# Performance work log

Hardware: AMD Instinct MI355X
Metric: run time of the kernel (lower is better)

Reference implementation:

```python
import jax, jax.numpy as jnp
import numpy as np

N, E, F, H, ED, C, G = 50000, 800000, 86, 128, 16, 18, 64
NEG_SLOPE = 0.2


def setup_inputs() -> dict:
    key = jax.random.key(0)
    ks = jax.random.split(key, 20)
    s = 0.1
    return {
        "x": jax.random.normal(ks[0], (N, F), jnp.float32),
        "edge_index": jax.random.randint(ks[1], (2, E), 0, N, jnp.int32),
        "edge_attr": jax.random.normal(ks[2], (E, ED), jnp.float32),
        "batch": jnp.sort(jax.random.randint(ks[3], (N,), 0, G, jnp.int32)),
        # conv1 params (GATConv, heads=1): lin, lin_edge (no bias), att vectors, bias
        "W1": jax.random.normal(ks[4], (F, H), jnp.float32) * s,
        "We1": jax.random.normal(ks[5], (ED, H), jnp.float32) * s,
        "as1": jax.random.normal(ks[6], (H,), jnp.float32) * s,
        "ad1": jax.random.normal(ks[7], (H,), jnp.float32) * s,
        "ae1": jax.random.normal(ks[8], (H,), jnp.float32) * s,
        "b1": jnp.zeros((H,), jnp.float32),
        # conv2 params
        "W2": jax.random.normal(ks[9], (H, H), jnp.float32) * s,
        "We2": jax.random.normal(ks[10], (ED, H), jnp.float32) * s,
        "as2": jax.random.normal(ks[11], (H,), jnp.float32) * s,
        "ad2": jax.random.normal(ks[12], (H,), jnp.float32) * s,
        "ae2": jax.random.normal(ks[13], (H,), jnp.float32) * s,
        "b2": jnp.zeros((H,), jnp.float32),
        # final classifier
        "Wl": jax.random.normal(ks[14], (H, C), jnp.float32) * s,
        "bl": jnp.zeros((C,), jnp.float32),
    }


def gat_conv(x, edge_attr, src, dst, W, We, a_src, a_dst, a_edge, bias):
    h = x @ W                                   # [N, H]
    e = edge_attr @ We                          # [E, H]
    # per-edge attention logits: a_src.h_j + a_dst.h_i + a_edge.e
    alpha = (h @ a_src)[src] + (h @ a_dst)[dst] + e @ a_edge   # [E]
    alpha = jax.nn.leaky_relu(alpha, NEG_SLOPE)
    # segment softmax over incoming edges of each destination node
    m = jax.ops.segment_max(alpha, dst, num_segments=N)
    ex = jnp.exp(alpha - m[dst])
    denom = jax.ops.segment_sum(ex, dst, num_segments=N)
    w = ex / jnp.maximum(denom[dst], 1e-16)     # [E]
    out = jax.ops.segment_sum(h[src] * w[:, None], dst, num_segments=N)
    return out + bias


def reference(x, edge_index, edge_attr, batch,
              W1, We1, as1, ad1, ae1, b1,
              W2, We2, as2, ad2, ae2, b2,
              Wl, bl):
    src, dst = edge_index[0], edge_index[1]
    h = jax.nn.relu(gat_conv(x, edge_attr, src, dst, W1, We1, as1, ad1, ae1, b1))
    h = jax.nn.relu(gat_conv(h, edge_attr, src, dst, W2, We2, as2, ad2, ae2, b2))
    pooled = jax.ops.segment_max(h, batch, num_segments=G)      # [G, H] global max pool
    pooled = jnp.where(jnp.isfinite(pooled), pooled, 0.0)       # guard empty graphs
    logits = pooled @ Wl + bl                                   # [G, C]
    return jax.nn.log_softmax(logits, axis=-1)
```

## Files before the change

kernel.cpp:

```cpp
#include <hip/hip_runtime.h>
#include <math.h>

#define N_NODES 50000
#define N_EDGES 800000
#define F_IN    86
#define H_DIM   128
#define ED_DIM  16
#define C_CLS   18
#define G_GRAPHS 64
#define NEG_SLOPE 0.2f
#define SCAN_BLOCKS ((N_NODES + 255) / 256)
#define EB_BLOCKS ((N_EDGES + 255) / 256)
#define GB_BLOCKS ((N_NODES + 63) / 64)

typedef _Float16 h2v   __attribute__((ext_vector_type(2)));
typedef _Float16 half8 __attribute__((ext_vector_type(8)));
typedef float    f4v   __attribute__((ext_vector_type(4)));

__device__ __forceinline__ void atomicMaxFloat(float* addr, float val) {
    if (val >= 0.0f) atomicMax((int*)addr, __float_as_int(val));
    else             atomicMin((unsigned int*)addr, __float_as_uint(val));
}

__global__ void prep(int* __restrict__ cnt, float* __restrict__ pooled,
                     const float* __restrict__ We1, const float* __restrict__ ae1,
                     const float* __restrict__ We2, const float* __restrict__ ae2,
                     float* __restrict__ ve1, float* __restrict__ ve2) {
    int b = blockIdx.x, t = threadIdx.x;
    if (b < SCAN_BLOCKS) {
        int i = b * 256 + t;
        if (i < N_NODES) cnt[i] = 0;
    } else {
        if (t < ED_DIM) {
            float s = 0.f;
            for (int h = 0; h < H_DIM; ++h) s += We1[t * H_DIM + h] * ae1[h];
            ve1[t] = s;
        } else if (t < 2 * ED_DIM) {
            int j = t - ED_DIM;
            float s = 0.f;
            for (int h = 0; h < H_DIM; ++h) s += We2[j * H_DIM + h] * ae2[h];
            ve2[j] = s;
        }
        for (int i = t; i < G_GRAPHS * H_DIM; i += 256) pooled[i] = 0.f;
    }
}

__global__ void hist_rank_dots(const int* __restrict__ dst, int* __restrict__ cnt,
                               unsigned short* __restrict__ rank,
                               const float* __restrict__ ea,
                               const float* __restrict__ ve1, const float* __restrict__ ve2,
                               unsigned int* __restrict__ dotp) {
    int e = blockIdx.x * blockDim.x + threadIdx.x;
    if (e >= N_EDGES) return;
    int r = atomicAdd(&cnt[dst[e]], 1);
    rank[e] = (unsigned short)r;
    const float4* p = (const float4*)(ea + (size_t)e * ED_DIM);
    float4 v0 = p[0], v1 = p[1], v2 = p[2], v3 = p[3];
    float s1 = v0.x*ve1[0] + v0.y*ve1[1] + v0.z*ve1[2] + v0.w*ve1[3]
             + v1.x*ve1[4] + v1.y*ve1[5] + v1.z*ve1[6] + v1.w*ve1[7]
             + v2.x*ve1[8] + v2.y*ve1[9] + v2.z*ve1[10] + v2.w*ve1[11]
             + v3.x*ve1[12] + v3.y*ve1[13] + v3.z*ve1[14] + v3.w*ve1[15];
    float s2 = v0.x*ve2[0] + v0.y*ve2[1] + v0.z*ve2[2] + v0.w*ve2[3]
             + v1.x*ve2[4] + v1.y*ve2[5] + v1.z*ve2[6] + v1.w*ve2[7]
             + v2.x*ve2[8] + v2.y*ve2[9] + v2.z*ve2[10] + v2.w*ve2[11]
             + v3.x*ve2[12] + v3.y*ve2[13] + v3.z*ve2[14] + v3.w*ve2[15];
    h2v dv;
    dv.x = (_Float16)s1;
    dv.y = (_Float16)s2;
    dotp[e] = __builtin_bit_cast(unsigned int, dv);
}

__global__ void scan1(const int* __restrict__ cnt, int* __restrict__ excl,
                      int* __restrict__ bsum) {
    __shared__ int s[256];
    int tid = threadIdx.x;
    int i = blockIdx.x * 256 + tid;
    int v = (i < N_NODES) ? cnt[i] : 0;
    s[tid] = v;
    __syncthreads();
    for (int o = 1; o < 256; o <<= 1) {
        int t = (tid >= o) ? s[tid - o] : 0;
        __syncthreads();
        s[tid] += t;
        __syncthreads();
    }
    if (i < N_NODES) excl[i] = s[tid] - v;
    if (tid == 255) bsum[blockIdx.x] = s[255];
}

__global__ void scan23(const int* __restrict__ excl, const int* __restrict__ bsum,
                       int* __restrict__ row_ptr) {
    __shared__ int s[256];
    int tid = threadIdx.x;
    int v = (tid < SCAN_BLOCKS) ? bsum[tid] : 0;
    s[tid] = v;
    __syncthreads();
    for (int o = 1; o < 256; o <<= 1) {
        int t = (tid >= o) ? s[tid - o] : 0;
        __syncthreads();
        s[tid] += t;
        __syncthreads();
    }
    int boff = s[blockIdx.x] - bsum[blockIdx.x];
    int i = blockIdx.x * 256 + tid;
    if (i < N_NODES) row_ptr[i] = excl[i] + boff;
    if (i == 0) row_ptr[N_NODES] = N_EDGES;
}

__global__ void scatter_lite(const int* __restrict__ src, const int* __restrict__ dst,
                             const int* __restrict__ row_ptr,
                             const unsigned short* __restrict__ rank,
                             const unsigned int* __restrict__ dotp,
                             int2* __restrict__ perm) {
    int e = blockIdx.x * blockDim.x + threadIdx.x;
    if (e >= N_EDGES) return;
    int pos = row_ptr[dst[e]] + rank[e];
    perm[pos] = make_int2(src[e], (int)dotp[e]);
}

#define KP1 104
__global__ __launch_bounds__(256)
void gemm1(const float* __restrict__ in, const float* __restrict__ W,
           const float* __restrict__ a_s, const float* __restrict__ a_d,
           _Float16* __restrict__ hout, float* __restrict__ hs, float* __restrict__ hd) {
    __shared__ __attribute__((aligned(16))) _Float16 Asm[64 * KP1];
    __shared__ __attribute__((aligned(16))) _Float16 Bsm[128 * KP1];
    __shared__ float sdots[64][2][2];
    int tid = threadIdx.x;
    int n0 = blockIdx.x * 64;

    const float2* in2 = (const float2*)(in + (size_t)n0 * F_IN);
    for (int idx = tid; idx < 64 * (F_IN / 2); idx += 256) {
        int r = idx / (F_IN / 2), k2 = idx - r * (F_IN / 2);
        float2 v = (n0 + r < N_NODES) ? in2[idx] : make_float2(0.f, 0.f);
        Asm[r * KP1 + 2 * k2]     = (_Float16)v.x;
        Asm[r * KP1 + 2 * k2 + 1] = (_Float16)v.y;
    }
    for (int idx = tid; idx < 64 * (96 - F_IN); idx += 256) {
        int r = idx / (96 - F_IN), k = F_IN + idx - r * (96 - F_IN);
        Asm[r * KP1 + k] = (_Float16)0.f;
    }
    const float4* W4 = (const float4*)W;
    for (int idx = tid; idx < F_IN * 32; idx += 256) {
        float4 v = W4[idx];
        int k = idx >> 5, n = (idx & 31) * 4;
        Bsm[(n + 0) * KP1 + k] = (_Float16)v.x;
        Bsm[(n + 1) * KP1 + k] = (_Float16)v.y;
        Bsm[(n + 2) * KP1 + k] = (_Float16)v.z;
        Bsm[(n + 3) * KP1 + k] = (_Float16)v.w;
    }
    for (int idx = tid; idx < 128 * (96 - F_IN); idx += 256) {
        int n = idx / (96 - F_IN), k = F_IN + idx - n * (96 - F_IN);
        Bsm[n * KP1 + k] = (_Float16)0.f;
    }
    __syncthreads();

    int wave = tid >> 6, lane = tid & 63;
    int wm = (wave & 1) * 32, wn = (wave >> 1) * 64;
    int m16 = lane & 15, quad = lane >> 4;

    f4v acc[2][4];
#pragma unroll
    for (int t = 0; t < 2; ++t)
#pragma unroll
        for (int c = 0; c < 4; ++c) acc[t][c] = (f4v){0.f, 0.f, 0.f, 0.f};

#pragma unroll
    for (int kk = 0; kk < 96 / 32; ++kk) {
        int koff = kk * 32 + quad * 8;
        half8 a0 = *(const half8*)&Asm[(wm + m16) * KP1 + koff];
        half8 a1 = *(const half8*)&Asm[(wm + 16 + m16) * KP1 + koff];
#pragma unroll
        for (int c = 0; c < 4; ++c) {
            half8 b = *(const half8*)&Bsm[(wn + c * 16 + m16) * KP1 + koff];
            acc[0][c] = __builtin_amdgcn_mfma_f32_16x16x32_f16(a0, b, acc[0][c], 0, 0, 0);
            acc[1][c] = __builtin_amdgcn_mfma_f32_16x16x32_f16(a1, b, acc[1][c], 0, 0, 0);
        }
    }

    float asv[4], adv[4];
#pragma unroll
    for (int c = 0; c < 4; ++c) {
        asv[c] = a_s[wn + c * 16 + m16];
        adv[c] = a_d[wn + c * 16 + m16];
    }
#pragma unroll
    for (int t = 0; t < 2; ++t)
#pragma unroll
        for (int r = 0; r < 4; ++r) {
            float ps = 0.f, pd = 0.f;
#pragma unroll
            for (int c = 0; c < 4; ++c) {
                float v = acc[t][c][r];
                ps += v * asv[c];
                pd += v * adv[c];
            }
#pragma unroll
            for (int o = 1; o < 16; o <<= 1) {
                ps += __shfl_xor(ps, o);
                pd += __shfl_xor(pd, o);
            }
            if (m16 == 0) {
                int row = wm + t * 16 + quad * 4 + r;
                sdots[row][wn >> 6][0] = ps;
                sdots[row][wn >> 6][1] = pd;
            }
        }
#pragma unroll
    for (int t = 0; t < 2; ++t)
#pragma unroll
        for (int c = 0; c < 4; ++c)
#pragma unroll
            for (int r = 0; r < 4; ++r) {
                int row = n0 + wm + t * 16 + quad * 4 + r;
                if (row < N_NODES)
                    hout[(size_t)row * H_DIM + wn + c * 16 + m16] = (_Float16)acc[t][c][r];
            }
    __syncthreads();
    if (tid < 64) {
        int row = n0 + tid;
        if (row < N_NODES) {
            hs[row] = sdots[tid][0][0] + sdots[tid][1][0];
            hd[row] = sdots[tid][0][1] + sdots[tid][1][1];
        }
    }
}

#define KP2 136
__global__ __launch_bounds__(256)
void gemm2(const _Float16* __restrict__ in, const float* __restrict__ W,
           const float* __restrict__ a_s, const float* __restrict__ a_d,
           _Float16* __restrict__ hout, float* __restrict__ hs, float* __restrict__ hd) {
    __shared__ __attribute__((aligned(16))) _Float16 Asm[64 * KP2];
    __shared__ __attribute__((aligned(16))) _Float16 Bsm[128 * KP2];
    __shared__ float sdots[64][2][2];
    int tid = threadIdx.x;
    int n0 = blockIdx.x * 64;

    const half8* in8 = (const half8*)(in + (size_t)n0 * H_DIM);
    for (int idx = tid; idx < 64 * 16; idx += 256) {
        int r = idx >> 4, k8 = idx & 15;
        half8 v = (n0 + r < N_NODES) ? in8[idx]
                                     : (half8){0, 0, 0, 0, 0, 0, 0, 0};
        *(half8*)&Asm[r * KP2 + k8 * 8] = v;
    }
    const float4* W4 = (const float4*)W;
    for (int idx = tid; idx < 128 * 32; idx += 256) {
        float4 v = W4[idx];
        int k = idx >> 5, n = (idx & 31) * 4;
        Bsm[(n + 0) * KP2 + k] = (_Float16)v.x;
        Bsm[(n + 1) * KP2 + k] = (_Float16)v.y;
        Bsm[(n + 2) * KP2 + k] = (_Float16)v.z;
        Bsm[(n + 3) * KP2 + k] = (_Float16)v.w;
    }
    __syncthreads();

    int wave = tid >> 6, lane = tid & 63;
    int wm = (wave & 1) * 32, wn = (wave >> 1) * 64;
    int m16 = lane & 15, quad = lane >> 4;

    f4v acc[2][4];
#pragma unroll
    for (int t = 0; t < 2; ++t)
#pragma unroll
        for (int c = 0; c < 4; ++c) acc[t][c] = (f4v){0.f, 0.f, 0.f, 0.f};

#pragma unroll
    for (int kk = 0; kk < 128 / 32; ++kk) {
        int koff = kk * 32 + quad * 8;
        half8 a0 = *(const half8*)&Asm[(wm + m16) * KP2 + koff];
        half8 a1 = *(const half8*)&Asm[(wm + 16 + m16) * KP2 + koff];
#pragma unroll
        for (int c = 0; c < 4; ++c) {
            half8 b = *(const half8*)&Bsm[(wn + c * 16 + m16) * KP2 + koff];
            acc[0][c] = __builtin_amdgcn_mfma_f32_16x16x32_f16(a0, b, acc[0][c], 0, 0, 0);
            acc[1][c] = __builtin_amdgcn_mfma_f32_16x16x32_f16(a1, b, acc[1][c], 0, 0, 0);
        }
    }

    float asv[4], adv[4];
#pragma unroll
    for (int c = 0; c < 4; ++c) {
        asv[c] = a_s[wn + c * 16 + m16];
        adv[c] = a_d[wn + c * 16 + m16];
    }
#pragma unroll
    for (int t = 0; t < 2; ++t)
#pragma unroll
        for (int r = 0; r < 4; ++r) {
            float ps = 0.f, pd = 0.f;
#pragma unroll
            for (int c = 0; c < 4; ++c) {
                float v = acc[t][c][r];
                ps += v * asv[c];
                pd += v * adv[c];
            }
#pragma unroll
            for (int o = 1; o < 16; o <<= 1) {
                ps += __shfl_xor(ps, o);
                pd += __shfl_xor(pd, o);
            }
            if (m16 == 0) {
                int row = wm + t * 16 + quad * 4 + r;
                sdots[row][wn >> 6][0] = ps;
                sdots[row][wn >> 6][1] = pd;
            }
        }
#pragma unroll
    for (int t = 0; t < 2; ++t)
#pragma unroll
        for (int c = 0; c < 4; ++c)
#pragma unroll
            for (int r = 0; r < 4; ++r) {
                int row = n0 + wm + t * 16 + quad * 4 + r;
                if (row < N_NODES)
                    hout[(size_t)row * H_DIM + wn + c * 16 + m16] = (_Float16)acc[t][c][r];
            }
    __syncthreads();
    if (tid < 64) {
        int row = n0 + tid;
        if (row < N_NODES) {
            hs[row] = sdots[tid][0][0] + sdots[tid][1][0];
            hd[row] = sdots[tid][0][1] + sdots[tid][1][1];
        }
    }
}

template<int DOT, bool POOL>
__global__ void gat_node(const int* __restrict__ row_ptr, const int2* __restrict__ perm,
                         const float* __restrict__ hs, const float* __restrict__ hd,
                         const _Float16* __restrict__ h, const float* __restrict__ bias,
                         _Float16* __restrict__ out,
                         const int* __restrict__ batch, float* __restrict__ pooled) {
    __shared__ float smax[H_DIM];
    __shared__ int sg[4];
    int tid = threadIdx.x;
    if (POOL) {
        if (tid < H_DIM) smax[tid] = 0.f;
        __syncthreads();
    }
    int n = blockIdx.x * 4 + (tid >> 6);
    int lane = tid & 63;
    int q = lane >> 4, m = lane & 15;
    int r0 = row_ptr[n], r1 = row_ptr[n + 1];
    float hdn = hd[n];

    float acc[8];
#pragma unroll
    for (int k = 0; k < 8; ++k) acc[k] = 0.f;
    float denl = 0.f;

    for (int c = r0; c < r1; c += 64) {
        int i = c + lane;
        float w = 0.f;
        int s = 0;
        if (i < r1) {
            int2 p = perm[i];
            s = p.x;
            h2v dv = __builtin_bit_cast(h2v, p.y);
            float dotv = (DOT == 1) ? (float)dv.x : (float)dv.y;
            float t = hs[s] + hdn + dotv;
            t = (t > 0.f) ? t : NEG_SLOPE * t;
            w = __expf(t);
        }
        denl += w;
        int lim = min(64, r1 - c);
        int njj = (lim + 7) >> 3;
        for (int jj = 0; jj < njj; ++jj) {
            int j1 = (jj << 3) + q;
            int j2 = j1 + 4;
            float w1 = __shfl(w, j1);
            int   s1 = __shfl(s, j1);
            float w2 = __shfl(w, j2);
            int   s2 = __shfl(s, j2);
            half8 v1 = *(const half8*)&h[(size_t)s1 * H_DIM + m * 8];
            half8 v2 = *(const half8*)&h[(size_t)s2 * H_DIM + m * 8];
#pragma unroll
            for (int k = 0; k < 8; ++k) acc[k] += w1 * (float)v1[k];
#pragma unroll
            for (int k = 0; k < 8; ++k) acc[k] += w2 * (float)v2[k];
        }
    }
#pragma unroll
    for (int k = 0; k < 8; ++k) {
        acc[k] += __shfl_xor(acc[k], 16);
        acc[k] += __shfl_xor(acc[k], 32);
    }
    float den = denl;
#pragma unroll
    for (int o = 32; o > 0; o >>= 1) den += __shfl_xor(den, o);
    float inv = 1.f / fmaxf(den, 1e-16f);

    float rv[8];
    if (q == 0) {
        float4 b0 = ((const float4*)bias)[2 * m];
        float4 b1 = ((const float4*)bias)[2 * m + 1];
        rv[0] = fmaxf(acc[0] * inv + b0.x, 0.f);
        rv[1] = fmaxf(acc[1] * inv + b0.y, 0.f);
        rv[2] = fmaxf(acc[2] * inv + b0.z, 0.f);
        rv[3] = fmaxf(acc[3] * inv + b0.w, 0.f);
        rv[4] = fmaxf(acc[4] * inv + b1.x, 0.f);
        rv[5] = fmaxf(acc[5] * inv + b1.y, 0.f);
        rv[6] = fmaxf(acc[6] * inv + b1.z, 0.f);
        rv[7] = fmaxf(acc[7] * inv + b1.w, 0.f);
    }

    if (!POOL) {
        if (q == 0) {
            half8 ov;
#pragma unroll
            for (int k = 0; k < 8; ++k) ov[k] = (_Float16)rv[k];
            *(half8*)&out[(size_t)n * H_DIM + m * 8] = ov;
        }
    } else {
        int g = batch[n];
        if (lane == 0) sg[tid >> 6] = g;
        if (q == 0) {
#pragma unroll
            for (int k = 0; k < 8; ++k)
                atomicMax((int*)&smax[m * 8 + k], __float_as_int(rv[k]));
        }
        __syncthreads();
        if (sg[0] == sg[3]) {
            if (tid < H_DIM)
                atomicMaxFloat(&pooled[sg[0] * H_DIM + tid], smax[tid]);
        } else {
            if (q == 0) {
#pragma unroll
                for (int k = 0; k < 8; ++k)
                    atomicMaxFloat(&pooled[g * H_DIM + m * 8 + k], rv[k]);
            }
        }
    }
}

__global__ void final_logits(const float* __restrict__ pooled, const float* __restrict__ Wl,
                             const float* __restrict__ bl, float* __restrict__ outp) {
    int g = threadIdx.x;
    if (g >= G_GRAPHS) return;
    float lg[C_CLS];
#pragma unroll
    for (int c = 0; c < C_CLS; ++c) lg[c] = bl[c];
    for (int k = 0; k < H_DIM; ++k) {
        float v = pooled[g * H_DIM + k];
#pragma unroll
        for (int c = 0; c < C_CLS; ++c) lg[c] += v * Wl[k * C_CLS + c];
    }
    float mx = lg[0];
#pragma unroll
    for (int c = 1; c < C_CLS; ++c) mx = fmaxf(mx, lg[c]);
    float se = 0.f;
#pragma unroll
    for (int c = 0; c < C_CLS; ++c) se += expf(lg[c] - mx);
    float lse = logf(se);
#pragma unroll
    for (int c = 0; c < C_CLS; ++c) outp[g * C_CLS + c] = lg[c] - mx - lse;
}

extern "C" void kernel_launch(void* const* d_in, const int* in_sizes, int n_in,
                              void* d_out, int out_size, void* d_ws, size_t ws_size,
                              hipStream_t stream) {
    const float* x     = (const float*)d_in[0];
    const int*   eidx  = (const int*)d_in[1];
    const float* ea    = (const float*)d_in[2];
    const int*   batch = (const int*)d_in[3];
    const float* W1  = (const float*)d_in[4];
    const float* We1 = (const float*)d_in[5];
    const float* as1 = (const float*)d_in[6];
    const float* ad1 = (const float*)d_in[7];
    const float* ae1 = (const float*)d_in[8];
    const float* b1  = (const float*)d_in[9];
    const float* W2  = (const float*)d_in[10];
    const float* We2 = (const float*)d_in[11];
    const float* as2 = (const float*)d_in[12];
    const float* ad2 = (const float*)d_in[13];
    const float* ae2 = (const float*)d_in[14];
    const float* b2  = (const float*)d_in[15];
    const float* Wl  = (const float*)d_in[16];
    const float* bl  = (const float*)d_in[17];
    float* outp = (float*)d_out;

    const int* src = eidx;
    const int* dst = eidx + N_EDGES;

    char* wsb = (char*)d_ws;
    size_t off = 0;
    auto alloc = [&](size_t bytes) { char* p = wsb + off; off += (bytes + 255) & ~(size_t)255; return p; };
    _Float16* h    = (_Float16*)alloc((size_t)N_NODES * H_DIM * 2);
    _Float16* A2   = (_Float16*)alloc((size_t)N_NODES * H_DIM * 2);
    int2*  perm    = (int2*)alloc((size_t)N_EDGES * 8);
    unsigned short* rank = (unsigned short*)alloc((size_t)N_EDGES * 2);
    unsigned int* dotp = (unsigned int*)alloc((size_t)N_EDGES * 4);
    float* hs      = (float*)alloc(N_NODES * 4);
    float* hd      = (float*)alloc(N_NODES * 4);
    int*   row_ptr = (int*)alloc((N_NODES + 1) * 4);
    int*   cnt     = (int*)alloc(N_NODES * 4);
    int*   excl    = (int*)alloc(N_NODES * 4);
    int*   bsum    = (int*)alloc(SCAN_BLOCKS * 4);
    float* pooled  = (float*)alloc(G_GRAPHS * H_DIM * 4);
    float* ve1     = (float*)alloc(16 * 4);
    float* ve2     = (float*)alloc(16 * 4);

    const int NB4 = (N_NODES + 3) / 4;

    prep<<<SCAN_BLOCKS + 1, 256, 0, stream>>>(cnt, pooled, We1, ae1, We2, ae2, ve1, ve2);
    hist_rank_dots<<<EB_BLOCKS, 256, 0, stream>>>(dst, cnt, rank, ea, ve1, ve2, dotp);
    scan1<<<SCAN_BLOCKS, 256, 0, stream>>>(cnt, excl, bsum);
    scan23<<<SCAN_BLOCKS, 256, 0, stream>>>(excl, bsum, row_ptr);
    scatter_lite<<<EB_BLOCKS, 256, 0, stream>>>(src, dst, row_ptr, rank, dotp, perm);

    gemm1<<<GB_BLOCKS, 256, 0, stream>>>(x, W1, as1, ad1, h, hs, hd);
    gat_node<1, false><<<NB4, 256, 0, stream>>>(row_ptr, perm, hs, hd, h, b1, A2,
                                                batch, pooled);

    gemm2<<<GB_BLOCKS, 256, 0, stream>>>(A2, W2, as2, ad2, h, hs, hd);
    gat_node<2, true><<<NB4, 256, 0, stream>>>(row_ptr, perm, hs, hd, h, b2, nullptr,
                                               batch, pooled);

    final_logits<<<1, 64, 0, stream>>>(pooled, Wl, bl, outp);
}
```

Before: 314.5 us.

## Fuse layer-1 GAT aggregation into the layer-2 GEMM kernel

Layer-1 attention aggregation now runs inside the layer-2 GEMM kernel. Each 512-thread block aggregates 32 nodes straight into shared memory and then multiplies them by W2 with MFMA, so the fp16 intermediate A2 is no longer written to and read back from global memory, and one launch disappears. The pool kernel also drops its per-element shared atomics in favour of per-wave smax slots followed by a max reduction. In exchange, each block now re-converts the full 128x128 W2 into shared memory for only 32 rows instead of 64, and the large LDS footprint with 512-thread blocks may reduce occupancy for the latency-bound gather phase.

```diff
diff --git a/kernel.cpp b/kernel.cpp
--- a/kernel.cpp
+++ b/kernel.cpp
@@ -12,6 +12,7 @@
 #define SCAN_BLOCKS ((N_NODES + 255) / 256)
 #define EB_BLOCKS ((N_EDGES + 255) / 256)
 #define GB_BLOCKS ((N_NODES + 63) / 64)
+#define FB_BLOCKS ((N_NODES + 31) / 32)
 
 typedef _Float16 h2v   __attribute__((ext_vector_type(2)));
 typedef _Float16 half8 __attribute__((ext_vector_type(8)));
@@ -20,6 +21,73 @@
 __device__ __forceinline__ void atomicMaxFloat(float* addr, float val) {
     if (val >= 0.0f) atomicMax((int*)addr, __float_as_int(val));
     else             atomicMin((unsigned int*)addr, __float_as_uint(val));
+}
+
+template<int DOT>
+__device__ __forceinline__ void gat_one_node(
+    int n, const int* __restrict__ row_ptr, const int2* __restrict__ perm,
+    const float* __restrict__ hs, const float* __restrict__ hd,
+    const _Float16* __restrict__ h, const float* __restrict__ bias,
+    int lane, int q, int m, float rv[8]) {
+    int r0 = row_ptr[n], r1 = row_ptr[n + 1];
+    float hdn = hd[n];
+    float acc[8];
+#pragma unroll
+    for (int k = 0; k < 8; ++k) acc[k] = 0.f;
+    float denl = 0.f;
+
+    for (int c = r0; c < r1; c += 64) {
+        int i = c + lane;
+        float w = 0.f;
+        int s = 0;
+        if (i < r1) {
+            int2 p = perm[i];
+            s = p.x;
+            h2v dv = __builtin_bit_cast(h2v, p.y);
+            float dotv = (DOT == 1) ? (float)dv.x : (float)dv.y;
+            float t = hs[s] + hdn + dotv;
+            t = (t > 0.f) ? t : NEG_SLOPE * t;
+            w = __expf(t);
+        }
+        denl += w;
+        int lim = min(64, r1 - c);
+        int njj = (lim + 7) >> 3;
+        for (int jj = 0; jj < njj; ++jj) {
+            int j1 = (jj << 3) + q;
+            int j2 = j1 + 4;
+            float w1 = __shfl(w, j1);
+            int   s1 = __shfl(s, j1);
+            float w2 = __shfl(w, j2);
+            int   s2 = __shfl(s, j2);
+            half8 v1 = *(const half8*)&h[(size_t)s1 * H_DIM + m * 8];
+            half8 v2 = *(const half8*)&h[(size_t)s2 * H_DIM + m * 8];
+#pragma unroll
+            for (int k = 0; k < 8; ++k) acc[k] += w1 * (float)v1[k];
+#pragma unroll
+            for (int k = 0; k < 8; ++k) acc[k] += w2 * (float)v2[k];
+        }
+    }
+#pragma unroll
+    for (int k = 0; k < 8; ++k) {
+        acc[k] += __shfl_xor(acc[k], 16);
+        acc[k] += __shfl_xor(acc[k], 32);
+    }
+    float den = denl;
+#pragma unroll
+    for (int o = 32; o > 0; o >>= 1) den += __shfl_xor(den, o);
+    float inv = 1.f / fmaxf(den, 1e-16f);
+    if (q == 0) {
+        float4 b0 = ((const float4*)bias)[2 * m];
+        float4 b1 = ((const float4*)bias)[2 * m + 1];
+        rv[0] = fmaxf(acc[0] * inv + b0.x, 0.f);
+        rv[1] = fmaxf(acc[1] * inv + b0.y, 0.f);
+        rv[2] = fmaxf(acc[2] * inv + b0.z, 0.f);
+        rv[3] = fmaxf(acc[3] * inv + b0.w, 0.f);
+        rv[4] = fmaxf(acc[4] * inv + b1.x, 0.f);
+        rv[5] = fmaxf(acc[5] * inv + b1.y, 0.f);
+        rv[6] = fmaxf(acc[6] * inv + b1.z, 0.f);
+        rv[7] = fmaxf(acc[7] * inv + b1.w, 0.f);
+    }
 }
 
 __global__ void prep(int* __restrict__ cnt, float* __restrict__ pooled,
@@ -227,25 +295,24 @@
 }
 
 #define KP2 136
-__global__ __launch_bounds__(256)
-void gemm2(const _Float16* __restrict__ in, const float* __restrict__ W,
-           const float* __restrict__ a_s, const float* __restrict__ a_d,
-           _Float16* __restrict__ hout, float* __restrict__ hs, float* __restrict__ hd) {
-    __shared__ __attribute__((aligned(16))) _Float16 Asm[64 * KP2];
+__global__ __launch_bounds__(512)
+void gat1_gemm2(const int* __restrict__ row_ptr, const int2* __restrict__ perm,
+                const float* __restrict__ hs1, const float* __restrict__ hd1,
+                const _Float16* __restrict__ h1, const float* __restrict__ b1,
+                const float* __restrict__ W2,
+                const float* __restrict__ as2, const float* __restrict__ ad2,
+                _Float16* __restrict__ hout, float* __restrict__ hs2,
+                float* __restrict__ hd2) {
+    __shared__ __attribute__((aligned(16))) _Float16 Asm[32 * KP2];
     __shared__ __attribute__((aligned(16))) _Float16 Bsm[128 * KP2];
-    __shared__ float sdots[64][2][2];
+    __shared__ float sdots[32][4][2];
     int tid = threadIdx.x;
-    int n0 = blockIdx.x * 64;
-
-    const half8* in8 = (const half8*)(in + (size_t)n0 * H_DIM);
-    for (int idx = tid; idx < 64 * 16; idx += 256) {
-        int r = idx >> 4, k8 = idx & 15;
-        half8 v = (n0 + r < N_NODES) ? in8[idx]
-                                     : (half8){0, 0, 0, 0, 0, 0, 0, 0};
-        *(half8*)&Asm[r * KP2 + k8 * 8] = v;
-    }
-    const float4* W4 = (const float4*)W;
-    for (int idx = tid; idx < 128 * 32; idx += 256) {
+    int n0 = blockIdx.x * 32;
+    int wv = tid >> 6, lane = tid & 63;
+    int q = lane >> 4, m = lane & 15;
+
+    const float4* W4 = (const float4*)W2;
+    for (int idx = tid; idx < 128 * 32; idx += 512) {
         float4 v = W4[idx];
         int k = idx >> 5, n = (idx & 31) * 4;
         Bsm[(n + 0) * KP2 + k] = (_Float16)v.x;
@@ -253,183 +320,110 @@
         Bsm[(n + 2) * KP2 + k] = (_Float16)v.z;
         Bsm[(n + 3) * KP2 + k] = (_Float16)v.w;
     }
-    __syncthreads();
-
-    int wave = tid >> 6, lane = tid & 63;
-    int wm = (wave & 1) * 32, wn = (wave >> 1) * 64;
-    int m16 = lane & 15, quad = lane >> 4;
-
-    f4v acc[2][4];
-#pragma unroll
-    for (int t = 0; t < 2; ++t)
-#pragma unroll
-        for (int c = 0; c < 4; ++c) acc[t][c] = (f4v){0.f, 0.f, 0.f, 0.f};
-
-#pragma unroll
-    for (int kk = 0; kk < 128 / 32; ++kk) {
-        int koff = kk * 32 + quad * 8;
-        half8 a0 = *(const half8*)&Asm[(wm + m16) * KP2 + koff];
-        half8 a1 = *(const half8*)&Asm[(wm + 16 + m16) * KP2 + koff];
-#pragma unroll
-        for (int c = 0; c < 4; ++c) {
-            half8 b = *(const half8*)&Bsm[(wn + c * 16 + m16) * KP2 + koff];
-            acc[0][c] = __builtin_amdgcn_mfma_f32_16x16x32_f16(a0, b, acc[0][c], 0, 0, 0);
-            acc[1][c] = __builtin_amdgcn_mfma_f32_16x16x32_f16(a1, b, acc[1][c], 0, 0, 0);
-        }
-    }
-
-    float asv[4], adv[4];
-#pragma unroll
-    for (int c = 0; c < 4; ++c) {
-        asv[c] = a_s[wn + c * 16 + m16];
-        adv[c] = a_d[wn + c * 16 + m16];
-    }
-#pragma unroll
-    for (int t = 0; t < 2; ++t)
+
+    for (int t = 0; t < 4; ++t) {
+        int n = n0 + wv * 4 + t;
+        if (n < N_NODES) {
+            float rv[8];
+            gat_one_node<1>(n, row_ptr, perm, hs1, hd1, h1, b1, lane, q, m, rv);
+            if (q == 0) {
+                half8 ov;
+#pragma unroll
+                for (int k = 0; k < 8; ++k) ov[k] = (_Float16)rv[k];
+                *(half8*)&Asm[(wv * 4 + t) * KP2 + m * 8] = ov;
+            }
+        } else if (q == 0) {
+            *(half8*)&Asm[(wv * 4 + t) * KP2 + m * 8] = (half8){0,0,0,0,0,0,0,0};
+        }
+    }
+    __syncthreads();
+
+    int wm = (wv & 1) * 16, wn = (wv >> 1) * 32;
+    f4v acc[2];
+    acc[0] = (f4v){0.f, 0.f, 0.f, 0.f};
+    acc[1] = (f4v){0.f, 0.f, 0.f, 0.f};
+#pragma unroll
+    for (int kk = 0; kk < 4; ++kk) {
+        int koff = kk * 32 + q * 8;
+        half8 a = *(const half8*)&Asm[(wm + m) * KP2 + koff];
+#pragma unroll
+        for (int c = 0; c < 2; ++c) {
+            half8 b = *(const half8*)&Bsm[(wn + c * 16 + m) * KP2 + koff];
+            acc[c] = __builtin_amdgcn_mfma_f32_16x16x32_f16(a, b, acc[c], 0, 0, 0);
+        }
+    }
+
+    float asv[2], adv[2];
+#pragma unroll
+    for (int c = 0; c < 2; ++c) {
+        asv[c] = as2[wn + c * 16 + m];
+        adv[c] = ad2[wn + c * 16 + m];
+    }
+#pragma unroll
+    for (int r = 0; r < 4; ++r) {
+        float ps = acc[0][r] * asv[0] + acc[1][r] * asv[1];
+        float pd = acc[0][r] * adv[0] + acc[1][r] * adv[1];
+#pragma unroll
+        for (int o = 1; o < 16; o <<= 1) {
+            ps += __shfl_xor(ps, o);
+            pd += __shfl_xor(pd, o);
+        }
+        if (m == 0) {
+            sdots[wm + q * 4 + r][wv >> 1][0] = ps;
+            sdots[wm + q * 4 + r][wv >> 1][1] = pd;
+        }
+    }
+#pragma unroll
+    for (int c = 0; c < 2; ++c)
 #pragma unroll
         for (int r = 0; r < 4; ++r) {
-            float ps = 0.f, pd = 0.f;
-#pragma unroll
-            for (int c = 0; c < 4; ++c) {
-                float v = acc[t][c][r];
-                ps += v * asv[c];
-                pd += v * adv[c];
-            }
-#pragma unroll
-            for (int o = 1; o < 16; o <<= 1) {
-                ps += __shfl_xor(ps, o);
-                pd += __shfl_xor(pd, o);
-            }
-            if (m16 == 0) {
-                int row = wm + t * 16 + quad * 4 + r;
-                sdots[row][wn >> 6][0] = ps;
-                sdots[row][wn >> 6][1] = pd;
-            }
-        }
-#pragma unroll
-    for (int t = 0; t < 2; ++t)
-#pragma unroll
-        for (int c = 0; c < 4; ++c)
-#pragma unroll
-            for (int r = 0; r < 4; ++r) {
-                int row = n0 + wm + t * 16 + quad * 4 + r;
-                if (row < N_NODES)
-                    hout[(size_t)row * H_DIM + wn + c * 16 + m16] = (_Float16)acc[t][c][r];
-            }
-    __syncthreads();
-    if (tid < 64) {
+            int row = n0 + wm + q * 4 + r;
+            if (row < N_NODES)
+                hout[(size_t)row * H_DIM + wn + c * 16 + m] = (_Float16)acc[c][r];
+        }
+    __syncthreads();
+    if (tid < 32) {
         int row = n0 + tid;
         if (row < N_NODES) {
-            hs[row] = sdots[tid][0][0] + sdots[tid][1][0];
-            hd[row] = sdots[tid][0][1] + sdots[tid][1][1];
-        }
-    }
-}
-
-template<int DOT, bool POOL>
-__global__ void gat_node(const int* __restrict__ row_ptr, const int2* __restrict__ perm,
+            hs2[row] = sdots[tid][0][0] + sdots[tid][1][0]
+                     + sdots[tid][2][0] + sdots[tid][3][0];
+            hd2[row] = sdots[tid][0][1] + sdots[tid][1][1]
+                     + sdots[tid][2][1] + sdots[tid][3][1];
+        }
+    }
+}
+
+__global__ void gat_pool(const int* __restrict__ row_ptr, const int2* __restrict__ perm,
                          const float* __restrict__ hs, const float* __restrict__ hd,
                          const _Float16* __restrict__ h, const float* __restrict__ bias,
-                         _Float16* __restrict__ out,
                          const int* __restrict__ batch, float* __restrict__ pooled) {
-    __shared__ float smax[H_DIM];
+    __shared__ float smax4[4][H_DIM];
     __shared__ int sg[4];
     int tid = threadIdx.x;
-    if (POOL) {
-        if (tid < H_DIM) smax[tid] = 0.f;
-        __syncthreads();
-    }
-    int n = blockIdx.x * 4 + (tid >> 6);
-    int lane = tid & 63;
-    int q = lane >> 4, m = lane & 15;
-    int r0 = row_ptr[n], r1 = row_ptr[n + 1];
-    float hdn = hd[n];
-
-    float acc[8];
-#pragma unroll
-    for (int k = 0; k < 8; ++k) acc[k] = 0.f;
-    float denl = 0.f;
-
-    for (int c = r0; c < r1; c += 64) {
-        int i = c + lane;
-        float w = 0.f;
-        int s = 0;
-        if (i < r1) {
-            int2 p = perm[i];
-            s = p.x;
-            h2v dv = __builtin_bit_cast(h2v, p.y);
-            float dotv = (DOT == 1) ? (float)dv.x : (float)dv.y;
-            float t = hs[s] + hdn + dotv;
-            t = (t > 0.f) ? t : NEG_SLOPE * t;
-            w = __expf(t);
-        }
-        denl += w;
-        int lim = min(64, r1 - c);
-        int njj = (lim + 7) >> 3;
-        for (int jj = 0; jj < njj; ++jj) {
-            int j1 = (jj << 3) + q;
-            int j2 = j1 + 4;
-            float w1 = __shfl(w, j1);
-            int   s1 = __shfl(s, j1);
-            float w2 = __shfl(w, j2);
-            int   s2 = __shfl(s, j2);
-            half8 v1 = *(const half8*)&h[(size_t)s1 * H_DIM + m * 8];
-            half8 v2 = *(const half8*)&h[(size_t)s2 * H_DIM + m * 8];
-#pragma unroll
-            for (int k = 0; k < 8; ++k) acc[k] += w1 * (float)v1[k];
-#pragma unroll
-            for (int k = 0; k < 8; ++k) acc[k] += w2 * (float)v2[k];
-        }
-    }
-#pragma unroll
-    for (int k = 0; k < 8; ++k) {
-        acc[k] += __shfl_xor(acc[k], 16);
-        acc[k] += __shfl_xor(acc[k], 32);
-    }
-    float den = denl;
-#pragma unroll
-    for (int o = 32; o > 0; o >>= 1) den += __shfl_xor(den, o);
-    float inv = 1.f / fmaxf(den, 1e-16f);
-
+    int wv = tid >> 6;
+    int n = blockIdx.x * 4 + wv;
+    int lane = tid & 63, q = lane >> 4, m = lane & 15;
     float rv[8];
+    gat_one_node<2>(n, row_ptr, perm, hs, hd, h, bias, lane, q, m, rv);
+    int g = batch[n];
+    if (lane == 0) sg[wv] = g;
     if (q == 0) {
-        float4 b0 = ((const float4*)bias)[2 * m];
-        float4 b1 = ((const float4*)bias)[2 * m + 1];
-        rv[0] = fmaxf(acc[0] * inv + b0.x, 0.f);
-        rv[1] = fmaxf(acc[1] * inv + b0.y, 0.f);
-        rv[2] = fmaxf(acc[2] * inv + b0.z, 0.f);
-        rv[3] = fmaxf(acc[3] * inv + b0.w, 0.f);
-        rv[4] = fmaxf(acc[4] * inv + b1.x, 0.f);
-        rv[5] = fmaxf(acc[5] * inv + b1.y, 0.f);
-        rv[6] = fmaxf(acc[6] * inv + b1.z, 0.f);
-        rv[7] = fmaxf(acc[7] * inv + b1.w, 0.f);
-    }
-
-    if (!POOL) {
+#pragma unroll
+        for (int k = 0; k < 8; ++k) smax4[wv][k * 16 + m] = rv[k];
+    }
+    __syncthreads();
+    if (sg[0] == sg[3]) {
+        if (tid < H_DIM) {
+            int p = (tid & 7) * 16 + (tid >> 3);
+            float v = fmaxf(fmaxf(smax4[0][p], smax4[1][p]),
+                            fmaxf(smax4[2][p], smax4[3][p]));
+            atomicMaxFloat(&pooled[sg[0] * H_DIM + tid], v);
+        }
+    } else {
         if (q == 0) {
-            half8 ov;
-#pragma unroll
-            for (int k = 0; k < 8; ++k) ov[k] = (_Float16)rv[k];
-            *(half8*)&out[(size_t)n * H_DIM + m * 8] = ov;
-        }
-    } else {
-        int g = batch[n];
-        if (lane == 0) sg[tid >> 6] = g;
-        if (q == 0) {
 #pragma unroll
             for (int k = 0; k < 8; ++k)
-                atomicMax((int*)&smax[m * 8 + k], __float_as_int(rv[k]));
-        }
-        __syncthreads();
-        if (sg[0] == sg[3]) {
-            if (tid < H_DIM)
-                atomicMaxFloat(&pooled[sg[0] * H_DIM + tid], smax[tid]);
-        } else {
-            if (q == 0) {
-#pragma unroll
-                for (int k = 0; k < 8; ++k)
-                    atomicMaxFloat(&pooled[g * H_DIM + m * 8 + k], rv[k]);
-            }
+                atomicMaxFloat(&pooled[g * H_DIM + m * 8 + k], rv[k]);
         }
     }
 }
@@ -486,13 +480,15 @@
     char* wsb = (char*)d_ws;
     size_t off = 0;
     auto alloc = [&](size_t bytes) { char* p = wsb + off; off += (bytes + 255) & ~(size_t)255; return p; };
-    _Float16* h    = (_Float16*)alloc((size_t)N_NODES * H_DIM * 2);
-    _Float16* A2   = (_Float16*)alloc((size_t)N_NODES * H_DIM * 2);
+    _Float16* h1   = (_Float16*)alloc((size_t)N_NODES * H_DIM * 2);
+    _Float16* h2   = (_Float16*)alloc((size_t)N_NODES * H_DIM * 2);
     int2*  perm    = (int2*)alloc((size_t)N_EDGES * 8);
     unsigned short* rank = (unsigned short*)alloc((size_t)N_EDGES * 2);
     unsigned int* dotp = (unsigned int*)alloc((size_t)N_EDGES * 4);
-    float* hs      = (float*)alloc(N_NODES * 4);
-    float* hd      = (float*)alloc(N_NODES * 4);
+    float* hs1     = (float*)alloc(N_NODES * 4);
+    float* hd1     = (float*)alloc(N_NODES * 4);
+    float* hs2     = (float*)alloc(N_NODES * 4);
+    float* hd2     = (float*)alloc(N_NODES * 4);
     int*   row_ptr = (int*)alloc((N_NODES + 1) * 4);
     int*   cnt     = (int*)alloc(N_NODES * 4);
     int*   excl    = (int*)alloc(N_NODES * 4);
@@ -509,13 +505,12 @@
     scan23<<<SCAN_BLOCKS, 256, 0, stream>>>(excl, bsum, row_ptr);
     scatter_lite<<<EB_BLOCKS, 256, 0, stream>>>(src, dst, row_ptr, rank, dotp, perm);
 
-    gemm1<<<GB_BLOCKS, 256, 0, stream>>>(x, W1, as1, ad1, h, hs, hd);
-    gat_node<1, false><<<NB4, 256, 0, stream>>>(row_ptr, perm, hs, hd, h, b1, A2,
-                                                batch, pooled);
-
-    gemm2<<<GB_BLOCKS, 256, 0, stream>>>(A2, W2, as2, ad2, h, hs, hd);
-    gat_node<2, true><<<NB4, 256, 0, stream>>>(row_ptr, perm, hs, hd, h, b2, nullptr,
-                                               batch, pooled);
+    gemm1<<<GB_BLOCKS, 256, 0, stream>>>(x, W1, as1, ad1, h1, hs1, hd1);
+
+    gat1_gemm2<<<FB_BLOCKS, 512, 0, stream>>>(row_ptr, perm, hs1, hd1, h1, b1,
+                                              W2, as2, ad2, h2, hs2, hd2);
+
+    gat_pool<<<NB4, 256, 0, stream>>>(row_ptr, perm, hs2, hd2, h2, b2, batch, pooled);
 
     final_logits<<<1, 64, 0, stream>>>(pooled, Wl, bl, outp);
 }
```

New measurement: 331.6 us. 1.05x slower.
